# Kernel tuning notes

Measured on AMD Instinct MI355X. Metric: run time of the kernel, lower is better.

## Reference

```python
import jax, jax.numpy as jnp
import numpy as np

B, S, E, H = 4, 2048, 2048, 16
D = E // H  # head_dim = 128


def setup_inputs() -> dict:
    key = jax.random.key(0)
    kx, kq, kk, kv = jax.random.split(key, 4)
    std = 1.0 / np.sqrt(E)
    return {
        "x": jax.random.normal(kx, (B, S, E), dtype=jnp.float32),
        "Wq": jax.random.normal(kq, (E, E), dtype=jnp.float32) * std,
        "Wk": jax.random.normal(kk, (E, E), dtype=jnp.float32) * std,
        "Wv": jax.random.normal(kv, (E, E), dtype=jnp.float32) * std,
    }


def reference(x, Wq, Wk, Wv):
    b, s, _ = x.shape
    # nn.Linear(bias=False): y = x @ W.T
    q = (x @ Wq.T).reshape(b, s, H, D).transpose(0, 2, 1, 3)  # [b,h,s,d]
    k = (x @ Wk.T).reshape(b, s, H, D).transpose(0, 2, 1, 3)
    v = (x @ Wv.T).reshape(b, s, H, D).transpose(0, 2, 1, 3)
    scale = jnp.sqrt(jnp.asarray(D, dtype=jnp.float32))
    scores = jnp.einsum("bhqd,bhkd->bhqk", q, k) / scale  # [b,h,s,s]
    causal = jnp.tril(jnp.ones((s, s), dtype=bool))
    scores = jnp.where(causal, scores, -jnp.inf)
    weights = jax.nn.softmax(scores, axis=-1)
    attn = jnp.einsum("bhqk,bhkd->bhqd", weights, v)  # [b,h,s,d]
    return attn
```

## Files before the change

### kernel.cpp

```cpp
#include <hip/hip_runtime.h>
#include <hip/hip_bf16.h>
#include <stdint.h>

#define Bdim 4
#define Sdim 2048
#define Edim 2048
#define Hdim 16
#define Ddim 128

typedef unsigned short u16;
typedef unsigned int u32;
typedef __attribute__((ext_vector_type(8))) short bf16x8;
typedef __attribute__((ext_vector_type(4))) float f32x4;
typedef __attribute__((ext_vector_type(16))) float f32x16;
typedef __attribute__((ext_vector_type(4))) unsigned short u16x4;
typedef __attribute__((ext_vector_type(2))) unsigned int u32x2;

__device__ inline u16 f2bf(float f) {
  union { float f; uint32_t u; } v; v.f = f;
  uint32_t u = v.u;
  return (u16)((u + 0x7FFFu + ((u >> 16) & 1u)) >> 16);
}

__device__ inline u32 pkbf(float lo, float hi) {
  float2 t; t.x = lo; t.y = hi;
  union { __hip_bfloat162 h2; u32 u; } cv;
  cv.h2 = __float22bfloat162_rn(t);
  return cv.u;
}

__device__ inline f32x4 mfma16(bf16x8 a, bf16x8 b, f32x4 c) {
  return __builtin_amdgcn_mfma_f32_16x16x32_bf16(a, b, c, 0, 0, 0);
}
__device__ inline f32x16 mfma32(bf16x8 a, bf16x8 b, f32x16 c) {
  return __builtin_amdgcn_mfma_f32_32x32x16_bf16(a, b, c, 0, 0, 0);
}

__device__ inline void load_lds16(const void* g, const void* l) {
  __builtin_amdgcn_global_load_lds(
      (__attribute__((address_space(1))) void*)(uintptr_t)g,
      (__attribute__((address_space(3))) void*)(uint32_t)(uintptr_t)l,
      16, 0, 0);
}

__global__ void cvt_kernel(const float* __restrict__ src, u16* __restrict__ dst,
                           int n4, float scale) {
  int i = blockIdx.x * blockDim.x + threadIdx.x;
  if (i < n4) {
    float4 f = ((const float4*)src)[i];
    u16x4 o = { f2bf(f.x * scale), f2bf(f.y * scale),
                f2bf(f.z * scale), f2bf(f.w * scale) };
    ((u16x4*)dst)[i] = o;
  }
}

__global__ void cvt_w_kernel(const float* __restrict__ Wq,
                             const float* __restrict__ Wk,
                             const float* __restrict__ Wv,
                             u16* __restrict__ dst, float qscale) {
  int i = blockIdx.x * blockDim.x + threadIdx.x;
  int seg = i >> 20;
  int off = i & 1048575;
  const float* src = seg == 0 ? Wq : (seg == 1 ? Wk : Wv);
  float sc = seg == 0 ? qscale : 1.0f;
  float4 f = ((const float4*)src)[off];
  u16x4 o = { f2bf(f.x * sc), f2bf(f.y * sc), f2bf(f.z * sc), f2bf(f.w * sc) };
  ((u16x4*)dst)[i] = o;
}

template <bool TRANSV>
__global__ __launch_bounds__(512, 2)
void gemm_nt(const u16* __restrict__ A, const u16* __restrict__ Bw,
             u16* __restrict__ C, int M, int N, int K) {
  __shared__ char lds[131072];

  const int tid = threadIdx.x;
  const int lane = tid & 63;
  const int w = tid >> 6;
  const int wm = w >> 2, wn = w & 3;
  const int bm = blockIdx.x, bn = blockIdx.y;
  const int NT = K >> 6;

  const int l15 = lane & 15;
  const int l4 = lane >> 4;
  const int h7 = l15 & 7;

  const int srow = lane >> 3;
  const int schunk = (lane & 7) ^ srow;

  const int ck0 = (l4 ^ h7) << 4;
  const int ck1 = ((4 + l4) ^ h7) << 4;
  const int arow0 = (wm * 16 + l15) * 128;
  const int brow0 = (wn * 16 + l15) * 128;

  const u16* Agp = A + (size_t)(bm * 256) * K;
  const u16* Bgp = Bw + (size_t)(bn * 256) * K;

  f32x4 acc[8][4];
#pragma unroll
  for (int m = 0; m < 8; ++m)
#pragma unroll
    for (int n = 0; n < 4; ++n)
      acc[m][n] = (f32x4){0.f, 0.f, 0.f, 0.f};

#define STG_A(hh, tt)                                                          \
  {                                                                            \
    char* d_ = lds + ((tt) & 1) * 65536 + (hh) * 16384;                        \
    _Pragma("unroll")                                                          \
    for (int i_ = 0; i_ < 2; ++i_)                                             \
      load_lds16(Agp + (size_t)((hh) * 128 + w * 8 + srow + i_ * 64) * K +     \
                     (tt) * 64 + schunk * 8,                                   \
                 d_ + (w * 8 + i_ * 64) * 128);                                \
  }
#define STG_B(hh, tt)                                                          \
  {                                                                            \
    char* d_ = lds + ((tt) & 1) * 65536 + 32768 + (hh) * 16384;                \
    _Pragma("unroll")                                                          \
    for (int i_ = 0; i_ < 2; ++i_)                                             \
      load_lds16(Bgp + (size_t)((hh) * 128 + w * 8 + srow + i_ * 64) * K +     \
                     (tt) * 64 + schunk * 8,                                   \
                 d_ + (w * 8 + i_ * 64) * 128);                                \
  }

  STG_A(0, 0); STG_B(0, 0); STG_B(1, 0); STG_A(1, 0);
  asm volatile("s_waitcnt vmcnt(0)" ::: "memory");
  __builtin_amdgcn_s_barrier();

  for (int t = 0; t < NT; ++t) {
    const char* bc = lds + (t & 1) * 65536;
    const bool pf = (t + 1 < NT);

    if (pf) STG_A(0, t + 1);
    bf16x8 a0[4][2], b0[2][2];
#pragma unroll
    for (int q = 0; q < 4; ++q) {
      a0[q][0] = *(const bf16x8*)(bc + arow0 + q * 4096 + ck0);
      a0[q][1] = *(const bf16x8*)(bc + arow0 + q * 4096 + ck1);
    }
#pragma unroll
    for (int n = 0; n < 2; ++n) {
      b0[n][0] = *(const bf16x8*)(bc + 32768 + brow0 + n * 8192 + ck0);
      b0[n][1] = *(const bf16x8*)(bc + 32768 + brow0 + n * 8192 + ck1);
    }
    __builtin_amdgcn_s_setprio(1);
#pragma unroll
    for (int q = 0; q < 4; ++q)
#pragma unroll
      for (int n = 0; n < 2; ++n) {
        acc[q][n] = mfma16(a0[q][0], b0[n][0], acc[q][n]);
        acc[q][n] = mfma16(a0[q][1], b0[n][1], acc[q][n]);
      }
    __builtin_amdgcn_s_setprio(0);
    asm volatile("s_waitcnt vmcnt(4)" ::: "memory");
    __builtin_amdgcn_s_barrier();

    if (pf) STG_B(0, t + 1);
    bf16x8 b1[2][2];
#pragma unroll
    for (int n = 0; n < 2; ++n) {
      b1[n][0] = *(const bf16x8*)(bc + 49152 + brow0 + n * 8192 + ck0);
      b1[n][1] = *(const bf16x8*)(bc + 49152 + brow0 + n * 8192 + ck1);
    }
    __builtin_amdgcn_s_setprio(1);
#pragma unroll
    for (int q = 0; q < 4; ++q)
#pragma unroll
      for (int n = 0; n < 2; ++n) {
        acc[q][n + 2] = mfma16(a0[q][0], b1[n][0], acc[q][n + 2]);
        acc[q][n + 2] = mfma16(a0[q][1], b1[n][1], acc[q][n + 2]);
      }
    __builtin_amdgcn_s_setprio(0);
    asm volatile("s_waitcnt vmcnt(4)" ::: "memory");
    __builtin_amdgcn_s_barrier();

    if (pf) STG_B(1, t + 1);
    bf16x8 a1[4][2];
#pragma unroll
    for (int q = 0; q < 4; ++q) {
      a1[q][0] = *(const bf16x8*)(bc + 16384 + arow0 + q * 4096 + ck0);
      a1[q][1] = *(const bf16x8*)(bc + 16384 + arow0 + q * 4096 + ck1);
    }
    __builtin_amdgcn_s_setprio(1);
#pragma unroll
    for (int q = 0; q < 4; ++q)
#pragma unroll
      for (int n = 0; n < 2; ++n) {
        acc[q + 4][n + 2] = mfma16(a1[q][0], b1[n][0], acc[q + 4][n + 2]);
        acc[q + 4][n + 2] = mfma16(a1[q][1], b1[n][1], acc[q + 4][n + 2]);
      }
    __builtin_amdgcn_s_setprio(0);
    asm volatile("s_waitcnt vmcnt(6)" ::: "memory");
    __builtin_amdgcn_s_barrier();

    if (pf) STG_A(1, t + 1);
    __builtin_amdgcn_s_setprio(1);
#pragma unroll
    for (int q = 0; q < 4; ++q)
#pragma unroll
      for (int n = 0; n < 2; ++n) {
        acc[q + 4][n] = mfma16(a1[q][0], b0[n][0], acc[q + 4][n]);
        acc[q + 4][n] = mfma16(a1[q][1], b0[n][1], acc[q + 4][n]);
      }
    __builtin_amdgcn_s_setprio(0);
    asm volatile("s_waitcnt vmcnt(4)" ::: "memory");
    __builtin_amdgcn_s_barrier();
  }
#undef STG_A
#undef STG_B

#pragma unroll
  for (int m = 0; m < 8; ++m)
#pragma unroll
    for (int n = 0; n < 4; ++n) {
      int r = bm * 256 + (m & 3) * 32 + wm * 16 + (m >> 2) * 128 + (l4 << 2);
      int c = bn * 256 + (n & 1) * 64 + wn * 16 + (n >> 1) * 128 + l15;
      if (!TRANSV) {
#pragma unroll
        for (int j = 0; j < 4; ++j)
          C[(size_t)(r + j) * N + c] = f2bf(acc[m][n][j]);
      } else {
        int h = c >> 7, d = c & 127;
        int b = r >> 11, s = r & 2047;
        u16x4 pk = { f2bf(acc[m][n][0]), f2bf(acc[m][n][1]),
                     f2bf(acc[m][n][2]), f2bf(acc[m][n][3]) };
        *(u16x4*)(C + ((size_t)((b * Hdim + h) * Ddim + d)) * Sdim + s) = pk;
      }
    }
}

__global__ __launch_bounds__(256)
void attn_kernel(const u16* __restrict__ Q, const u16* __restrict__ K,
                 const u16* __restrict__ Vt, float* __restrict__ O) {
  __shared__ u16 Ks[2][64 * 128];
  __shared__ u16 Vs[2][128 * 64];

  const int tid = threadIdx.x;
  const int lane = tid & 63;
  const int w = tid >> 6;
  const int l31 = lane & 31;
  const int hi = lane >> 5;

  const int bid = blockIdx.x;
  const int bh = bid & 63;
  const int qg = 15 - (bid >> 6);
  const int q0 = qg * 128;
  const int qw0 = q0 + w * 32;
  const int b = bh >> 4, h = bh & 15;

  const u16* Qb = Q + (size_t)b * Sdim * Edim + h * Ddim;
  const u16* Kb = K + (size_t)b * Sdim * Edim + h * Ddim;
  const u16* Vb = Vt + (size_t)bh * Ddim * Sdim;

  bf16x8 qf[8];
  {
    const u16* qrow = Qb + (size_t)(qw0 + l31) * Edim + hi * 8;
#pragma unroll
    for (int c = 0; c < 8; ++c) qf[c] = *(const bf16x8*)(qrow + c * 16);
  }

  f32x16 oacc[4];
#pragma unroll
  for (int d = 0; d < 4; ++d)
#pragma unroll
    for (int i = 0; i < 16; ++i) oacc[d][i] = 0.f;
  f32x16 lacc;
#pragma unroll
  for (int i = 0; i < 16; ++i) lacc[i] = 0.f;

  const short oneb = (short)0x3F80;
  const bf16x8 ones = {oneb, oneb, oneb, oneb, oneb, oneb, oneb, oneb};

  float m2 = -1e30f;
  const int qrel = qw0 + l31;

  const int nt = 2 * qg + 2;
  const int ntw = (qw0 + 31) / 64 + 1;

  const int krow_off = (lane >> 4);
  const int kchunk = lane & 15;
  const int vrow_off = (lane >> 3);
  const int vchunk = lane & 7;

#define STAGE(bufi, tt)                                                        \
  {                                                                            \
    const int kv0s = (tt) * 64;                                                \
    _Pragma("unroll")                                                          \
    for (int i = 0; i < 4; ++i) {                                              \
      const int rbase = w * 16 + i * 4;                                        \
      const int row = rbase + krow_off;                                        \
      const int cs = kchunk ^ (row & 15);                                      \
      load_lds16(Kb + (size_t)(kv0s + row) * Edim + cs * 8,                    \
                 &Ks[bufi][rbase * 128]);                                      \
    }                                                                          \
    _Pragma("unroll")                                                          \
    for (int i = 0; i < 4; ++i) {                                              \
      const int rbase = w * 32 + i * 8;                                        \
      const int row = rbase + vrow_off;                                        \
      const int cs = vchunk ^ (row & 7);                                       \
      load_lds16(Vb + (size_t)row * Sdim + kv0s + cs * 8,                      \
                 &Vs[bufi][rbase * 64]);                                       \
    }                                                                          \
  }

  STAGE(0, 0);
  __syncthreads();

  for (int t = 0; t < nt; ++t) {
    const int cur = t & 1;
    if (t + 1 < nt) STAGE(cur ^ 1, t + 1);

    if (t < ntw) {
      const int kv0 = t * 64;

      f32x16 sc0, sc1;
#pragma unroll
      for (int i = 0; i < 16; ++i) { sc0[i] = 0.f; sc1[i] = 0.f; }
#pragma unroll
      for (int c = 0; c < 8; ++c) {
        const int ch = c * 2 + hi;
        const int r0r = l31;
        const int r1r = 32 + l31;
        bf16x8 kf0 = *(const bf16x8*)&Ks[cur][r0r * 128 + (ch ^ (r0r & 15)) * 8];
        bf16x8 kf1 = *(const bf16x8*)&Ks[cur][r1r * 128 + (ch ^ (r1r & 15)) * 8];
        sc0 = mfma32(kf0, qf[c], sc0);
        sc1 = mfma32(kf1, qf[c], sc1);
      }

      float psc[32];
      float ma = -1e30f, mb = -1e30f, mc = -1e30f, md = -1e30f;
      if (kv0 + 64 > qw0) {
#pragma unroll
        for (int r = 0; r < 16; ++r) {
          const int cr = (r & 3) + 8 * (r >> 2) + 4 * hi;
          float v0 = (kv0 + cr <= qrel) ? sc0[r] : -1e30f;
          float v1 = (kv0 + 32 + cr <= qrel) ? sc1[r] : -1e30f;
          psc[r] = v0; psc[16 + r] = v1;
          if ((r & 3) == 0) { ma = fmaxf(fmaxf(ma, v0), v1); }
          else if ((r & 3) == 1) { mb = fmaxf(fmaxf(mb, v0), v1); }
          else if ((r & 3) == 2) { mc = fmaxf(fmaxf(mc, v0), v1); }
          else { md = fmaxf(fmaxf(md, v0), v1); }
        }
      } else {
#pragma unroll
        for (int r = 0; r < 16; ++r) {
          float v0 = sc0[r];
          float v1 = sc1[r];
          psc[r] = v0; psc[16 + r] = v1;
          if ((r & 3) == 0) { ma = fmaxf(fmaxf(ma, v0), v1); }
          else if ((r & 3) == 1) { mb = fmaxf(fmaxf(mb, v0), v1); }
          else if ((r & 3) == 2) { mc = fmaxf(fmaxf(mc, v0), v1); }
          else { md = fmaxf(fmaxf(md, v0), v1); }
        }
      }
      float mt = fmaxf(fmaxf(ma, mb), fmaxf(mc, md));
      u32x2 mx = __builtin_amdgcn_permlane32_swap(
          __float_as_uint(mt), __float_as_uint(mt), false, false);
      float mo = fmaxf(__uint_as_float(mx.x), __uint_as_float(mx.y));

      if (__any(mo - m2 > 8.0f)) {
        float mnew = fmaxf(m2, mo);
        float corr = __builtin_amdgcn_exp2f(m2 - mnew);
        m2 = mnew;
        lacc[0] *= corr;
#pragma unroll
        for (int d = 0; d < 4; ++d)
#pragma unroll
          for (int i = 0; i < 16; ++i) oacc[d][i] *= corr;
      }

#pragma unroll
      for (int r = 0; r < 32; ++r)
        psc[r] = __builtin_amdgcn_exp2f(psc[r] - m2);

      u32 pk[16];
#pragma unroll
      for (int i = 0; i < 16; ++i) pk[i] = pkbf(psc[2 * i], psc[2 * i + 1]);
      bf16x8 pa[4];
#pragma unroll
      for (int t2 = 0; t2 < 2; ++t2)
#pragma unroll
        for (int q2 = 0; q2 < 2; ++q2) {
          const int base = t2 * 8 + q2 * 4;
          u32x2 r0 = __builtin_amdgcn_permlane32_swap(pk[base + 0], pk[base + 2],
                                                      false, false);
          u32x2 r1 = __builtin_amdgcn_permlane32_swap(pk[base + 1], pk[base + 3],
                                                      false, false);
          union { u32 wv[4]; bf16x8 v; } cv;
          cv.wv[0] = r0.x; cv.wv[1] = r1.x; cv.wv[2] = r0.y; cv.wv[3] = r1.y;
          pa[t2 * 2 + q2] = cv.v;
        }

#pragma unroll
      for (int dblk = 0; dblk < 4; ++dblk) {
        const int row = dblk * 32 + l31;
#pragma unroll
        for (int ks = 0; ks < 4; ++ks) {
          const int ch = ks * 2 + hi;
          bf16x8 vf = *(const bf16x8*)&Vs[cur][row * 64 + (ch ^ (row & 7)) * 8];
          oacc[dblk] = mfma32(vf, pa[ks], oacc[dblk]);
        }
      }
#pragma unroll
      for (int ks = 0; ks < 4; ++ks) lacc = mfma32(ones, pa[ks], lacc);
    }

    __syncthreads();
  }
#undef STAGE

  float inv = 1.0f / lacc[0];
  float* Ob = O + ((size_t)bh * Sdim + qw0 + l31) * Ddim + hi * 4;
#pragma unroll
  for (int dblk = 0; dblk < 4; ++dblk)
#pragma unroll
    for (int g = 0; g < 4; ++g) {
      f32x4 o4 = { oacc[dblk][4 * g] * inv, oacc[dblk][4 * g + 1] * inv,
                   oacc[dblk][4 * g + 2] * inv, oacc[dblk][4 * g + 3] * inv };
      *(f32x4*)(Ob + dblk * 32 + g * 8) = o4;
    }
}

extern "C" void kernel_launch(void* const* d_in, const int* in_sizes, int n_in,
                              void* d_out, int out_size, void* d_ws, size_t ws_size,
                              hipStream_t stream) {
  const float* x  = (const float*)d_in[0];
  const float* Wq = (const float*)d_in[1];
  const float* Wk = (const float*)d_in[2];
  const float* Wv = (const float*)d_in[3];
  float* out = (float*)d_out;
  char* ws = (char*)d_ws;

  u16* xb  = (u16*)(ws);
  u16* wqb = (u16*)(ws + 33554432ull);
  u16* wkb = (u16*)(ws + 41943040ull);
  u16* wvb = (u16*)(ws + 50331648ull);
  u16* Qb  = (u16*)(ws + 58720256ull);
  u16* Kb  = (u16*)(ws + 92274688ull);
  u16* Vt  = (u16*)(ws + 125829120ull);

  const int nX = Bdim * Sdim * Edim;
  const int nW = Edim * Edim;
  const float K1SC = 0.08838834764831845f * 1.4426950408889634f;
  cvt_kernel<<<(nX / 4 + 255) / 256, 256, 0, stream>>>(x, xb, nX / 4, 1.0f);
  cvt_w_kernel<<<(3 * nW / 4 + 255) / 256, 256, 0, stream>>>(Wq, Wk, Wv, wqb, K1SC);

  dim3 g(Bdim * Sdim / 256, Edim / 256);
  gemm_nt<false><<<g, 512, 0, stream>>>(xb, wqb, Qb, Bdim * Sdim, Edim, Edim);
  gemm_nt<false><<<g, 512, 0, stream>>>(xb, wkb, Kb, Bdim * Sdim, Edim, Edim);
  gemm_nt<true ><<<g, 512, 0, stream>>>(xb, wvb, Vt, Bdim * Sdim, Edim, Edim);

  attn_kernel<<<Bdim * Hdim * (Sdim / 128), 256, 0, stream>>>(Qb, Kb, Vt, out);
}
```

Before: 362.7 us.

## Shrink attention KV tile from 64 to 32 keys per iteration

Halves the K/V tile staged per loop iteration in the flash-attention kernel, doubling the trip count and reworking the LDS swizzle, causal diagonal test and P-packing for a 32-key tile. Each warp handles 32 queries, so its diagonal now falls in a single tile and the per-warp masked waste shrinks. LDS use is halved, which may let more blocks share a CU. In exchange the kernel pays more barriers, more softmax max/rescale rounds and shorter MFMA chains per sync.

```diff
diff --git a/kernel.cpp b/kernel.cpp
--- a/kernel.cpp
+++ b/kernel.cpp
@@ -231,8 +231,8 @@
 __global__ __launch_bounds__(256)
 void attn_kernel(const u16* __restrict__ Q, const u16* __restrict__ K,
                  const u16* __restrict__ Vt, float* __restrict__ O) {
-  __shared__ u16 Ks[2][64 * 128];
-  __shared__ u16 Vs[2][128 * 64];
+  __shared__ u16 Ks[2][32 * 128];
+  __shared__ u16 Vs[2][128 * 32];
 
   const int tid = threadIdx.x;
   const int lane = tid & 63;
@@ -271,34 +271,34 @@
   const bf16x8 ones = {oneb, oneb, oneb, oneb, oneb, oneb, oneb, oneb};
 
   float m2 = -1e30f;
-  const int qrel = qw0 + l31;
-
-  const int nt = 2 * qg + 2;
-  const int ntw = (qw0 + 31) / 64 + 1;
-
-  const int krow_off = (lane >> 4);
+
+  const int nt = 4 * qg + 4;
+  const int tdiag = qw0 >> 5;
+  const int ntw = tdiag + 1;
+
+  const int krow_off = lane >> 4;
   const int kchunk = lane & 15;
-  const int vrow_off = (lane >> 3);
-  const int vchunk = lane & 7;
+  const int vrow_off = lane >> 2;
+  const int vchunk = lane & 3;
 
 #define STAGE(bufi, tt)                                                        \
   {                                                                            \
-    const int kv0s = (tt) * 64;                                                \
+    const int kv0s = (tt) * 32;                                                \
     _Pragma("unroll")                                                          \
-    for (int i = 0; i < 4; ++i) {                                              \
-      const int rbase = w * 16 + i * 4;                                        \
+    for (int i = 0; i < 2; ++i) {                                              \
+      const int rbase = w * 8 + i * 4;                                         \
       const int row = rbase + krow_off;                                        \
       const int cs = kchunk ^ (row & 15);                                      \
       load_lds16(Kb + (size_t)(kv0s + row) * Edim + cs * 8,                    \
                  &Ks[bufi][rbase * 128]);                                      \
     }                                                                          \
     _Pragma("unroll")                                                          \
-    for (int i = 0; i < 4; ++i) {                                              \
-      const int rbase = w * 32 + i * 8;                                        \
+    for (int i = 0; i < 2; ++i) {                                              \
+      const int rbase = w * 32 + i * 16;                                       \
       const int row = rbase + vrow_off;                                        \
-      const int cs = vchunk ^ (row & 7);                                       \
+      const int cs = vchunk ^ ((row >> 1) & 3);                                \
       load_lds16(Vb + (size_t)row * Sdim + kv0s + cs * 8,                      \
-                 &Vs[bufi][rbase * 64]);                                       \
+                 &Vs[bufi][rbase * 32]);                                       \
     }                                                                          \
   }
 
@@ -310,46 +310,38 @@
     if (t + 1 < nt) STAGE(cur ^ 1, t + 1);
 
     if (t < ntw) {
-      const int kv0 = t * 64;
-
-      f32x16 sc0, sc1;
-#pragma unroll
-      for (int i = 0; i < 16; ++i) { sc0[i] = 0.f; sc1[i] = 0.f; }
+      f32x16 sc;
+#pragma unroll
+      for (int i = 0; i < 16; ++i) sc[i] = 0.f;
 #pragma unroll
       for (int c = 0; c < 8; ++c) {
         const int ch = c * 2 + hi;
-        const int r0r = l31;
-        const int r1r = 32 + l31;
-        bf16x8 kf0 = *(const bf16x8*)&Ks[cur][r0r * 128 + (ch ^ (r0r & 15)) * 8];
-        bf16x8 kf1 = *(const bf16x8*)&Ks[cur][r1r * 128 + (ch ^ (r1r & 15)) * 8];
-        sc0 = mfma32(kf0, qf[c], sc0);
-        sc1 = mfma32(kf1, qf[c], sc1);
-      }
-
-      float psc[32];
+        bf16x8 kf = *(const bf16x8*)&Ks[cur][l31 * 128 + ((ch ^ (l31 & 15)) * 8)];
+        sc = mfma32(kf, qf[c], sc);
+      }
+
+      float psc[16];
       float ma = -1e30f, mb = -1e30f, mc = -1e30f, md = -1e30f;
-      if (kv0 + 64 > qw0) {
+      if (t == tdiag) {
 #pragma unroll
         for (int r = 0; r < 16; ++r) {
           const int cr = (r & 3) + 8 * (r >> 2) + 4 * hi;
-          float v0 = (kv0 + cr <= qrel) ? sc0[r] : -1e30f;
-          float v1 = (kv0 + 32 + cr <= qrel) ? sc1[r] : -1e30f;
-          psc[r] = v0; psc[16 + r] = v1;
-          if ((r & 3) == 0) { ma = fmaxf(fmaxf(ma, v0), v1); }
-          else if ((r & 3) == 1) { mb = fmaxf(fmaxf(mb, v0), v1); }
-          else if ((r & 3) == 2) { mc = fmaxf(fmaxf(mc, v0), v1); }
-          else { md = fmaxf(fmaxf(md, v0), v1); }
+          float v = (cr <= l31) ? sc[r] : -1e30f;
+          psc[r] = v;
+          if ((r & 3) == 0) ma = fmaxf(ma, v);
+          else if ((r & 3) == 1) mb = fmaxf(mb, v);
+          else if ((r & 3) == 2) mc = fmaxf(mc, v);
+          else md = fmaxf(md, v);
         }
       } else {
 #pragma unroll
         for (int r = 0; r < 16; ++r) {
-          float v0 = sc0[r];
-          float v1 = sc1[r];
-          psc[r] = v0; psc[16 + r] = v1;
-          if ((r & 3) == 0) { ma = fmaxf(fmaxf(ma, v0), v1); }
-          else if ((r & 3) == 1) { mb = fmaxf(fmaxf(mb, v0), v1); }
-          else if ((r & 3) == 2) { mc = fmaxf(fmaxf(mc, v0), v1); }
-          else { md = fmaxf(fmaxf(md, v0), v1); }
+          float v = sc[r];
+          psc[r] = v;
+          if ((r & 3) == 0) ma = fmaxf(ma, v);
+          else if ((r & 3) == 1) mb = fmaxf(mb, v);
+          else if ((r & 3) == 2) mc = fmaxf(mc, v);
+          else md = fmaxf(md, v);
         }
       }
       float mt = fmaxf(fmaxf(ma, mb), fmaxf(mc, md));
@@ -369,39 +361,37 @@
       }
 
 #pragma unroll
-      for (int r = 0; r < 32; ++r)
+      for (int r = 0; r < 16; ++r)
         psc[r] = __builtin_amdgcn_exp2f(psc[r] - m2);
 
-      u32 pk[16];
-#pragma unroll
-      for (int i = 0; i < 16; ++i) pk[i] = pkbf(psc[2 * i], psc[2 * i + 1]);
-      bf16x8 pa[4];
-#pragma unroll
-      for (int t2 = 0; t2 < 2; ++t2)
-#pragma unroll
-        for (int q2 = 0; q2 < 2; ++q2) {
-          const int base = t2 * 8 + q2 * 4;
-          u32x2 r0 = __builtin_amdgcn_permlane32_swap(pk[base + 0], pk[base + 2],
-                                                      false, false);
-          u32x2 r1 = __builtin_amdgcn_permlane32_swap(pk[base + 1], pk[base + 3],
-                                                      false, false);
-          union { u32 wv[4]; bf16x8 v; } cv;
-          cv.wv[0] = r0.x; cv.wv[1] = r1.x; cv.wv[2] = r0.y; cv.wv[3] = r1.y;
-          pa[t2 * 2 + q2] = cv.v;
-        }
+      u32 pk[8];
+#pragma unroll
+      for (int i = 0; i < 8; ++i) pk[i] = pkbf(psc[2 * i], psc[2 * i + 1]);
+      bf16x8 pa[2];
+#pragma unroll
+      for (int q2 = 0; q2 < 2; ++q2) {
+        const int base = q2 * 4;
+        u32x2 r0 = __builtin_amdgcn_permlane32_swap(pk[base + 0], pk[base + 2],
+                                                    false, false);
+        u32x2 r1 = __builtin_amdgcn_permlane32_swap(pk[base + 1], pk[base + 3],
+                                                    false, false);
+        union { u32 wv[4]; bf16x8 v; } cv;
+        cv.wv[0] = r0.x; cv.wv[1] = r1.x; cv.wv[2] = r0.y; cv.wv[3] = r1.y;
+        pa[q2] = cv.v;
+      }
 
 #pragma unroll
       for (int dblk = 0; dblk < 4; ++dblk) {
         const int row = dblk * 32 + l31;
 #pragma unroll
-        for (int ks = 0; ks < 4; ++ks) {
+        for (int ks = 0; ks < 2; ++ks) {
           const int ch = ks * 2 + hi;
-          bf16x8 vf = *(const bf16x8*)&Vs[cur][row * 64 + (ch ^ (row & 7)) * 8];
+          bf16x8 vf = *(const bf16x8*)&Vs[cur][row * 32 + ((ch ^ ((row >> 1) & 3)) * 8)];
           oacc[dblk] = mfma32(vf, pa[ks], oacc[dblk]);
         }
       }
 #pragma unroll
-      for (int ks = 0; ks < 4; ++ks) lacc = mfma32(ones, pa[ks], lacc);
+      for (int ks = 0; ks < 2; ++ks) lacc = mfma32(ones, pa[ks], lacc);
     }
 
     __syncthreads();
```

Result: slower. 389.3 us (+7.3%).
